# Performance work log

Hardware: AMD Instinct MI355X
Metric: run time of the kernel (lower is better)

The kernel has to match this reference:

```python
import jax, jax.numpy as jnp
import numpy as np

NUM_HEADS = 4

def setup_inputs() -> dict:
    key = jax.random.key(0)
    k1, k2, k3, k4 = jax.random.split(key, 4)
    B, N, D = 8, 768, 2048
    x = jax.random.normal(k1, (B, N, D), dtype=jnp.float32)
    s = 1.0 / np.sqrt(N)
    W_qk = jax.random.normal(k2, (N, N), dtype=jnp.float32) * s
    W_v = jax.random.normal(k3, (N, N), dtype=jnp.float32) * s
    W_out = jax.random.normal(k4, (N, N), dtype=jnp.float32) * s
    return {"x": x, "W_qk": W_qk, "W_v": W_v, "W_out": W_out}

def reference(x, W_qk, W_v, W_out):
    B, N, D = x.shape
    H = NUM_HEADS
    n = N // H
    y = jnp.swapaxes(x, 1, 2)                    # (B, D, N): attention over channels D
    qk = y @ W_qk.T                              # (B, D, N)
    v = y @ W_v.T                                # (B, D, N)
    # to heads: (B, D, N) -> (B, H, D, n)
    qk = jnp.swapaxes(qk.reshape(B, D, H, n), 1, 2)
    v = jnp.swapaxes(v.reshape(B, D, H, n), 1, 2)
    dot = jnp.einsum('bhdn,bhen->bhde', qk, qk)  # (B, H, D, D)
    q2 = jnp.sum(qk * qk, axis=-1)               # (B, H, D)
    # negative squared Euclidean distance logits: 2*q.k - ||q||^2 - ||k||^2
    logits = 2.0 * dot - q2[..., :, None] - q2[..., None, :]
    attn = jax.nn.softmax(logits, axis=-1)
    w = jnp.einsum('bhde,bhen->bhdn', attn, v)   # (B, H, D, n)
    # from heads: (B, H, D, n) -> (B, D, N)
    w = jnp.swapaxes(w, 1, 2).reshape(B, D, N)
    out = w @ W_out.T                            # (B, D, N)
    return jnp.swapaxes(out, 1, 2)               # (B, N, D)
```

## Files before the change

kernel.cpp:

```cpp
#include <hip/hip_runtime.h>
#include <stdint.h>

#define B_  8
#define N_  768
#define D_  2048
#define H_  4
#define HN  192

#define QROW 200
#define VROW 72
#define KTILE_B 25600
#define VTILE_B 27648

typedef unsigned short u16;
typedef float    f32x4 __attribute__((ext_vector_type(4)));
typedef __bf16   bf16x8 __attribute__((ext_vector_type(8)));
typedef uint32_t u32x4 __attribute__((ext_vector_type(4)));
typedef uint32_t u32x2 __attribute__((ext_vector_type(2)));

__device__ __forceinline__ u16 f2bf(float f) {
  uint32_t u = __builtin_bit_cast(uint32_t, f);
  u += 0x7fffu + ((u >> 16) & 1u);
  return (u16)(u >> 16);
}

typedef const __attribute__((address_space(1))) void* gas_ptr;
typedef __attribute__((address_space(3))) void* las_ptr;
__device__ __forceinline__ void gld16(const void* g, void* l) {
  __builtin_amdgcn_global_load_lds((gas_ptr)g, (las_ptr)l, 16, 0, 0);
}

__global__ __launch_bounds__(256) void transpose_x(const float* __restrict__ x,
                                                   u16* __restrict__ xt) {
  __shared__ float tile[64][65];
  const int d0 = blockIdx.x * 64;
  const int n0 = blockIdx.y * 64;
  const int b  = blockIdx.z;
  const int t   = threadIdx.x;
  const int col = t & 63;
  const int rb  = (t >> 6) * 16;
  const float* src = x + ((size_t)b * N_ + n0) * D_ + d0;
  #pragma unroll
  for (int i = 0; i < 16; i++)
    tile[rb + i][col] = src[(size_t)(rb + i) * D_ + col];
  __syncthreads();
  u16* dst = xt + ((size_t)b * D_ + d0) * N_ + n0;
  #pragma unroll
  for (int i = 0; i < 16; i++)
    dst[(size_t)(rb + i) * N_ + col] = f2bf(tile[col][rb + i]);
}

__global__ __launch_bounds__(256) void cvt_w(const float* __restrict__ a,
                                             const float* __restrict__ b,
                                             const float* __restrict__ c,
                                             u16* __restrict__ oa,
                                             u16* __restrict__ ob,
                                             u16* __restrict__ oc) {
  const float* src = (blockIdx.y == 0) ? a : ((blockIdx.y == 1) ? b : c);
  u16*         dst = (blockIdx.y == 0) ? oa : ((blockIdx.y == 1) ? ob : oc);
  const int i = (blockIdx.x * 256 + threadIdx.x) * 4;
  f32x4 v = *(const f32x4*)(src + i);
  u16 tmp[4];
  #pragma unroll
  for (int j = 0; j < 4; j++) tmp[j] = f2bf(v[j]);
  *(u32x2*)(dst + i) = *(u32x2*)tmp;
}

__global__ __launch_bounds__(256) void zero_q2(float* __restrict__ q2) {
  q2[blockIdx.x * 256 + threadIdx.x] = 0.f;
}

__global__ __launch_bounds__(256, 2) void qkv_gemm(const u16* __restrict__ xt,
                                                   const u16* __restrict__ wqk,
                                                   const u16* __restrict__ wv,
                                                   u16* __restrict__ qkb,
                                                   u16* __restrict__ vtb,
                                                   float* __restrict__ q2) {
  const int b     = blockIdx.z;
  const int dtile = blockIdx.x;
  const int d0    = dtile * 128;
  const int j0    = blockIdx.y * 128;
  const int tid  = threadIdx.x;
  const int wave = tid >> 6, lane = tid & 63;
  const int l15  = lane & 15, quad = lane >> 4;
  const int wm = wave >> 1, wn = wave & 1;

  __shared__ u16 At[128 * 32];
  __shared__ u16 Bq[128 * 32];
  __shared__ u16 Bv[128 * 32];

  const f32x4 fz = {0.f, 0.f, 0.f, 0.f};
  f32x4 accq[4][4];
  f32x4 accv[4][4];
  #pragma unroll
  for (int i = 0; i < 4; i++)
    #pragma unroll
    for (int j = 0; j < 4; j++) { accq[i][j] = fz; accv[i][j] = fz; }

  const int srow  = tid >> 2;
  const int sbyte = (tid & 3) * 16;
  const u16* ax = xt  + ((size_t)b * D_ + d0 + srow) * N_;
  const u16* bq = wqk + (size_t)(j0 + srow) * N_;
  const u16* bv = wv  + (size_t)(j0 + srow) * N_;

  for (int k0 = 0; k0 < N_; k0 += 32) {
    __syncthreads();
    #pragma unroll
    for (int c = 0; c < 2; c++) {
      gld16((const char*)(ax + (size_t)c * 64 * N_ + k0) + sbyte,
            (char*)At + c * 4096 + tid * 16);
      gld16((const char*)(bq + (size_t)c * 64 * N_ + k0) + sbyte,
            (char*)Bq + c * 4096 + tid * 16);
      gld16((const char*)(bv + (size_t)c * 64 * N_ + k0) + sbyte,
            (char*)Bv + c * 4096 + tid * 16);
    }
    __syncthreads();

    bf16x8 Af[4];
    #pragma unroll
    for (int mi = 0; mi < 4; mi++)
      Af[mi] = *(const bf16x8*)&At[(wm * 64 + mi * 16 + l15) * 32 + quad * 8];
    #pragma unroll
    for (int ni = 0; ni < 4; ni++) {
      bf16x8 Bqf = *(const bf16x8*)&Bq[(wn * 64 + ni * 16 + l15) * 32 + quad * 8];
      bf16x8 Bvf = *(const bf16x8*)&Bv[(wn * 64 + ni * 16 + l15) * 32 + quad * 8];
      #pragma unroll
      for (int mi = 0; mi < 4; mi++) {
        accq[ni][mi] = __builtin_amdgcn_mfma_f32_16x16x32_bf16(Bqf, Af[mi], accq[ni][mi], 0, 0, 0);
        accv[mi][ni] = __builtin_amdgcn_mfma_f32_16x16x32_bf16(Af[mi], Bvf, accv[mi][ni], 0, 0, 0);
      }
    }
  }

  const int h_w  = (j0 + wn * 64) / HN;
  const int jn_w = (j0 + wn * 64) % HN;
  const size_t bh = (size_t)b * H_ + h_w;

  #pragma unroll
  for (int md = 0; md < 4; md++) {
    float s = 0.f;
    #pragma unroll
    for (int nj = 0; nj < 4; nj++)
      #pragma unroll
      for (int r = 0; r < 4; r++) { float v = accq[nj][md][r]; s += v * v; }
    s += __shfl_xor(s, 16, 64);
    s += __shfl_xor(s, 32, 64);
    if (quad == 0)
      atomicAdd(&q2[bh * D_ + d0 + wm * 64 + md * 16 + l15], s);
  }

  u16* qtbase = qkb + bh * (size_t)(D_ * QROW);
  #pragma unroll
  for (int md = 0; md < 4; md++) {
    const size_t dro = (size_t)(d0 + wm * 64 + md * 16 + l15) * QROW;
    #pragma unroll
    for (int nj = 0; nj < 4; nj++) {
      u16 tmp[4];
      #pragma unroll
      for (int r = 0; r < 4; r++) tmp[r] = f2bf(accq[nj][md][r]);
      *(u32x2*)(qtbase + dro + jn_w + nj * 16 + quad * 4) = *(u32x2*)tmp;
    }
  }

  const int etile = dtile * 2 + wm;
  u16* vtbase = vtb + bh * (size_t)(32 * HN * VROW) + (size_t)etile * (HN * VROW);
  #pragma unroll
  for (int ni = 0; ni < 4; ni++) {
    const size_t jro = (size_t)(jn_w + ni * 16 + l15) * VROW;
    #pragma unroll
    for (int mi = 0; mi < 4; mi++) {
      u16 tmp[4];
      #pragma unroll
      for (int r = 0; r < 4; r++) tmp[r] = f2bf(accv[mi][ni][r]);
      *(u32x2*)(vtbase + jro + mi * 16 + quad * 4) = *(u32x2*)tmp;
    }
  }
}

__global__ __launch_bounds__(256, 2) void attn_kernel(const u16* __restrict__ qkb,
                                                      const u16* __restrict__ vtb,
                                                      const float* __restrict__ q2,
                                                      u16* __restrict__ wbuf) {
  const int bid  = blockIdx.x;
  const int bh   = (bid & 7) * 4 + (bid >> 7);
  const int dblk = (bid >> 3) & 15;
  const int b = bh >> 2, h = bh & 3;
  const int tid  = threadIdx.x;
  const int wave = tid >> 6, lane = tid & 63;
  const int l15  = lane & 15, quad = lane >> 4;

  __shared__ u16 Klds[64 * QROW];
  __shared__ u16 Vlds[HN * VROW];
  __shared__ u16 Plds[4][32][VROW];
  __shared__ float rsl[4][32];

  const u16* kg = qkb + (size_t)bh * (D_ * QROW);
  const u16* vg = vtb + (size_t)bh * (32 * HN * VROW);
  const float* q2g = q2 + (size_t)bh * D_;

  bf16x8 Qf[2][6];
  {
    const u16* qrow = kg + (size_t)(dblk * 128 + wave * 32 + l15) * QROW + quad * 8;
    #pragma unroll
    for (int nt = 0; nt < 2; nt++)
      #pragma unroll
      for (int f = 0; f < 6; f++)
        Qf[nt][f] = *(const bf16x8*)(qrow + (size_t)nt * 16 * QROW + f * 32);
  }
  float cd[2];
  cd[0] = q2g[dblk * 128 + wave * 32 + l15];
  cd[1] = q2g[dblk * 128 + wave * 32 + 16 + l15];

  const f32x4 fz = {0.f, 0.f, 0.f, 0.f};
  f32x4 O[2][12];
  #pragma unroll
  for (int mt = 0; mt < 2; mt++)
    #pragma unroll
    for (int c = 0; c < 12; c++) O[mt][c] = fz;
  float rsp[2] = {0.f, 0.f};

  for (int t = 0; t < 32; t++) {
    __syncthreads();
    {
      const char* ks = (const char*)kg + (size_t)t * KTILE_B;
      char* kd = (char*)Klds;
      for (int c = wave; c < 25; c += 4)
        gld16(ks + c * 1024 + lane * 16, kd + c * 1024 + lane * 16);
      const char* vs = (const char*)vg + (size_t)t * VTILE_B;
      char* vd = (char*)Vlds;
      for (int c = wave; c < 27; c += 4)
        gld16(vs + c * 1024 + lane * 16, vd + c * 1024 + lane * 16);
    }
    __syncthreads();

    #pragma unroll
    for (int et = 0; et < 4; et++) {
      bf16x8 Kf[6];
      #pragma unroll
      for (int f = 0; f < 6; f++)
        Kf[f] = *(const bf16x8*)&Klds[(et * 16 + l15) * QROW + f * 32 + quad * 8];
      f32x4 S0 = fz, S1 = fz;
      #pragma unroll
      for (int f = 0; f < 6; f++) {
        S0 = __builtin_amdgcn_mfma_f32_16x16x32_bf16(Kf[f], Qf[0][f], S0, 0, 0, 0);
        S1 = __builtin_amdgcn_mfma_f32_16x16x32_bf16(Kf[f], Qf[1][f], S1, 0, 0, 0);
      }
      const f32x4 ce = *(const f32x4*)&q2g[t * 64 + et * 16 + quad * 4];
      u16 pk0[4], pk1[4];
      #pragma unroll
      for (int r = 0; r < 4; r++) {
        float p0 = __expf(__builtin_fmaf(S0[r], 2.f, -(ce[r] + cd[0])));
        float p1 = __expf(__builtin_fmaf(S1[r], 2.f, -(ce[r] + cd[1])));
        rsp[0] += p0; rsp[1] += p1;
        pk0[r] = f2bf(p0); pk1[r] = f2bf(p1);
      }
      *(u32x2*)&Plds[wave][l15][et * 16 + quad * 4]      = *(u32x2*)pk0;
      *(u32x2*)&Plds[wave][16 + l15][et * 16 + quad * 4] = *(u32x2*)pk1;
    }

    #pragma unroll
    for (int kk = 0; kk < 2; kk++) {
      bf16x8 Pf0 = *(const bf16x8*)&Plds[wave][l15][kk * 32 + quad * 8];
      bf16x8 Pf1 = *(const bf16x8*)&Plds[wave][16 + l15][kk * 32 + quad * 8];
      #pragma unroll
      for (int c = 0; c < 12; c++) {
        bf16x8 Vf = *(const bf16x8*)&Vlds[(c * 16 + l15) * VROW + kk * 32 + quad * 8];
        O[0][c] = __builtin_amdgcn_mfma_f32_16x16x32_bf16(Pf0, Vf, O[0][c], 0, 0, 0);
        O[1][c] = __builtin_amdgcn_mfma_f32_16x16x32_bf16(Pf1, Vf, O[1][c], 0, 0, 0);
      }
    }
  }

  #pragma unroll
  for (int nt = 0; nt < 2; nt++) {
    float s = rsp[nt];
    s += __shfl_xor(s, 16, 64);
    s += __shfl_xor(s, 32, 64);
    if (quad == 0) rsl[wave][nt * 16 + l15] = s;
  }
  __builtin_amdgcn_s_waitcnt(0);
  #pragma unroll
  for (int mt = 0; mt < 2; mt++)
    #pragma unroll
    for (int r = 0; r < 4; r++) {
      const float inv = 1.f / rsl[wave][mt * 16 + quad * 4 + r];
      const int d = dblk * 128 + wave * 32 + mt * 16 + quad * 4 + r;
      u16* wrow = wbuf + ((size_t)b * D_ + d) * N_ + h * HN;
      #pragma unroll
      for (int c = 0; c < 12; c++)
        wrow[c * 16 + l15] = f2bf(O[mt][c][r] * inv);
    }
}

__global__ __launch_bounds__(256, 2) void out_gemm(const u16* __restrict__ wbuf,
                                                   const u16* __restrict__ wout,
                                                   float* __restrict__ outp) {
  const int b  = blockIdx.z;
  const int d0 = blockIdx.x * 128;
  const int i0 = blockIdx.y * 128;
  const int tid  = threadIdx.x;
  const int wave = tid >> 6, lane = tid & 63;
  const int l15  = lane & 15, quad = lane >> 4;
  const int wm = wave >> 1, wn = wave & 1;

  __shared__ u16 At[128 * 32];
  __shared__ u16 Bt[128 * 32];

  const f32x4 fz = {0.f, 0.f, 0.f, 0.f};
  f32x4 acc[4][4];
  #pragma unroll
  for (int i = 0; i < 4; i++)
    #pragma unroll
    for (int j = 0; j < 4; j++) acc[i][j] = fz;

  const int srow  = tid >> 2;
  const int sbyte = (tid & 3) * 16;
  const u16* ax = wbuf + ((size_t)b * D_ + d0 + srow) * N_;
  const u16* bw = wout + (size_t)(i0 + srow) * N_;

  for (int k0 = 0; k0 < N_; k0 += 32) {
    __syncthreads();
    #pragma unroll
    for (int c = 0; c < 2; c++) {
      gld16((const char*)(ax + (size_t)c * 64 * N_ + k0) + sbyte,
            (char*)At + c * 4096 + tid * 16);
      gld16((const char*)(bw + (size_t)c * 64 * N_ + k0) + sbyte,
            (char*)Bt + c * 4096 + tid * 16);
    }
    __syncthreads();

    bf16x8 Af[4];
    #pragma unroll
    for (int mi = 0; mi < 4; mi++)
      Af[mi] = *(const bf16x8*)&At[(wm * 64 + mi * 16 + l15) * 32 + quad * 8];
    #pragma unroll
    for (int ni = 0; ni < 4; ni++) {
      bf16x8 Bf = *(const bf16x8*)&Bt[(wn * 64 + ni * 16 + l15) * 32 + quad * 8];
      #pragma unroll
      for (int mi = 0; mi < 4; mi++)
        acc[mi][ni] = __builtin_amdgcn_mfma_f32_16x16x32_bf16(Af[mi], Bf, acc[mi][ni], 0, 0, 0);
    }
  }

  #pragma unroll
  for (int ni = 0; ni < 4; ni++) {
    float* orow = outp + ((size_t)b * N_ + i0 + wn * 64 + ni * 16 + l15) * D_
                + d0 + wm * 64 + quad * 4;
    #pragma unroll
    for (int mi = 0; mi < 4; mi++)
      *(f32x4*)(orow + mi * 16) = acc[mi][ni];
  }
}

extern "C" void kernel_launch(void* const* d_in, const int* in_sizes, int n_in,
                              void* d_out, int out_size, void* d_ws, size_t ws_size,
                              hipStream_t stream) {
  (void)in_sizes; (void)n_in; (void)out_size; (void)ws_size;
  const float* x    = (const float*)d_in[0];
  const float* Wqk  = (const float*)d_in[1];
  const float* Wv   = (const float*)d_in[2];
  const float* Wout = (const float*)d_in[3];
  float* outp = (float*)d_out;

  char* ws = (char*)d_ws;
  size_t off = 0;
  u16* xt   = (u16*)(ws + off); off += (size_t)B_ * D_ * N_ * 2;
  u16* qkb  = (u16*)(ws + off); off += (size_t)B_ * H_ * D_ * QROW * 2;
  u16* vtb  = (u16*)(ws + off); off += (size_t)B_ * H_ * 32 * HN * VROW * 2;
  float* q2 = (float*)(ws + off); off += (size_t)B_ * H_ * D_ * 4;
  u16* wqk_bf  = (u16*)(ws + off); off += (size_t)N_ * N_ * 2;
  u16* wv_bf   = (u16*)(ws + off); off += (size_t)N_ * N_ * 2;
  u16* wout_bf = (u16*)(ws + off); off += (size_t)N_ * N_ * 2;
  u16* wbuf = xt;

  transpose_x<<<dim3(D_ / 64, N_ / 64, B_), 256, 0, stream>>>(x, xt);
  cvt_w<<<dim3((N_ * N_) / (256 * 4), 3), 256, 0, stream>>>(Wqk, Wv, Wout, wqk_bf, wv_bf, wout_bf);
  zero_q2<<<dim3((B_ * H_ * D_) / 256), 256, 0, stream>>>(q2);
  qkv_gemm<<<dim3(D_ / 128, N_ / 128, B_), 256, 0, stream>>>(xt, wqk_bf, wv_bf, qkb, vtb, q2);
  attn_kernel<<<dim3((D_ / 128) * B_ * H_), 256, 0, stream>>>(qkb, vtb, q2, wbuf);
  out_gemm<<<dim3(D_ / 128, N_ / 128, B_), 256, 0, stream>>>(wbuf, wout_bf, outp);
}
```

Measured before the change: 303.8 us.

## Compute softmax row sums via MFMA with ones, use exp2 and hardware bf16 converts

Folds log2(e) into the precomputed squared norms and the logit scale, so the attention kernel can call the native exp2 instruction instead of expf. The per-lane running row-sum and its shuffle/LDS reduction are replaced by an extra MFMA of P against an all-ones fragment, which yields row sums directly in accumulator layout. Software bf16 rounding is replaced by hardware casts, and s_setprio is placed around the MFMA blocks to favour matrix-issue scheduling. This adds two MFMAs per k-step and computes the row sum from bf16-rounded probabilities, which slightly changes numerics.

```diff
diff --git a/kernel.cpp b/kernel.cpp
--- a/kernel.cpp
+++ b/kernel.cpp
@@ -12,16 +12,18 @@
 #define KTILE_B 25600
 #define VTILE_B 27648
 
+#define LOG2E 1.4426950408889634f
+#define C2    2.8853901617f
+
 typedef unsigned short u16;
 typedef float    f32x4 __attribute__((ext_vector_type(4)));
 typedef __bf16   bf16x8 __attribute__((ext_vector_type(8)));
+typedef __bf16   bf16x4 __attribute__((ext_vector_type(4)));
 typedef uint32_t u32x4 __attribute__((ext_vector_type(4)));
 typedef uint32_t u32x2 __attribute__((ext_vector_type(2)));
 
 __device__ __forceinline__ u16 f2bf(float f) {
-  uint32_t u = __builtin_bit_cast(uint32_t, f);
-  u += 0x7fffu + ((u >> 16) & 1u);
-  return (u16)(u >> 16);
+  return __builtin_bit_cast(u16, (__bf16)f);
 }
 
 typedef const __attribute__((address_space(1))) void* gas_ptr;
@@ -146,7 +148,7 @@
     s += __shfl_xor(s, 16, 64);
     s += __shfl_xor(s, 32, 64);
     if (quad == 0)
-      atomicAdd(&q2[bh * D_ + d0 + wm * 64 + md * 16 + l15], s);
+      atomicAdd(&q2[bh * D_ + d0 + wm * 64 + md * 16 + l15], s * LOG2E);
   }
 
   u16* qtbase = qkb + bh * (size_t)(D_ * QROW);
@@ -155,10 +157,10 @@
     const size_t dro = (size_t)(d0 + wm * 64 + md * 16 + l15) * QROW;
     #pragma unroll
     for (int nj = 0; nj < 4; nj++) {
-      u16 tmp[4];
-      #pragma unroll
-      for (int r = 0; r < 4; r++) tmp[r] = f2bf(accq[nj][md][r]);
-      *(u32x2*)(qtbase + dro + jn_w + nj * 16 + quad * 4) = *(u32x2*)tmp;
+      bf16x4 tmp;
+      #pragma unroll
+      for (int r = 0; r < 4; r++) tmp[r] = (__bf16)accq[nj][md][r];
+      *(bf16x4*)(qtbase + dro + jn_w + nj * 16 + quad * 4) = tmp;
     }
   }
 
@@ -169,10 +171,10 @@
     const size_t jro = (size_t)(jn_w + ni * 16 + l15) * VROW;
     #pragma unroll
     for (int mi = 0; mi < 4; mi++) {
-      u16 tmp[4];
-      #pragma unroll
-      for (int r = 0; r < 4; r++) tmp[r] = f2bf(accv[mi][ni][r]);
-      *(u32x2*)(vtbase + jro + mi * 16 + quad * 4) = *(u32x2*)tmp;
+      bf16x4 tmp;
+      #pragma unroll
+      for (int r = 0; r < 4; r++) tmp[r] = (__bf16)accv[mi][ni][r];
+      *(bf16x4*)(vtbase + jro + mi * 16 + quad * 4) = tmp;
     }
   }
 }
@@ -192,7 +194,6 @@
   __shared__ u16 Klds[64 * QROW];
   __shared__ u16 Vlds[HN * VROW];
   __shared__ u16 Plds[4][32][VROW];
-  __shared__ float rsl[4][32];
 
   const u16* kg = qkb + (size_t)bh * (D_ * QROW);
   const u16* vg = vtb + (size_t)bh * (32 * HN * VROW);
@@ -211,13 +212,19 @@
   cd[0] = q2g[dblk * 128 + wave * 32 + l15];
   cd[1] = q2g[dblk * 128 + wave * 32 + 16 + l15];
 
+  bf16x8 OnesF;
+  #pragma unroll
+  for (int j = 0; j < 8; j++) OnesF[j] = (__bf16)1.0f;
+
   const f32x4 fz = {0.f, 0.f, 0.f, 0.f};
   f32x4 O[2][12];
-  #pragma unroll
-  for (int mt = 0; mt < 2; mt++)
+  f32x4 Or[2];
+  #pragma unroll
+  for (int mt = 0; mt < 2; mt++) {
+    Or[mt] = fz;
     #pragma unroll
     for (int c = 0; c < 12; c++) O[mt][c] = fz;
-  float rsp[2] = {0.f, 0.f};
+  }
 
   for (int t = 0; t < 32; t++) {
     __syncthreads();
@@ -240,50 +247,48 @@
       for (int f = 0; f < 6; f++)
         Kf[f] = *(const bf16x8*)&Klds[(et * 16 + l15) * QROW + f * 32 + quad * 8];
       f32x4 S0 = fz, S1 = fz;
+      __builtin_amdgcn_s_setprio(1);
       #pragma unroll
       for (int f = 0; f < 6; f++) {
         S0 = __builtin_amdgcn_mfma_f32_16x16x32_bf16(Kf[f], Qf[0][f], S0, 0, 0, 0);
         S1 = __builtin_amdgcn_mfma_f32_16x16x32_bf16(Kf[f], Qf[1][f], S1, 0, 0, 0);
       }
+      __builtin_amdgcn_s_setprio(0);
       const f32x4 ce = *(const f32x4*)&q2g[t * 64 + et * 16 + quad * 4];
-      u16 pk0[4], pk1[4];
+      bf16x4 pb0, pb1;
       #pragma unroll
       for (int r = 0; r < 4; r++) {
-        float p0 = __expf(__builtin_fmaf(S0[r], 2.f, -(ce[r] + cd[0])));
-        float p1 = __expf(__builtin_fmaf(S1[r], 2.f, -(ce[r] + cd[1])));
-        rsp[0] += p0; rsp[1] += p1;
-        pk0[r] = f2bf(p0); pk1[r] = f2bf(p1);
+        float p0 = __builtin_amdgcn_exp2f(__builtin_fmaf(S0[r], C2, -(ce[r] + cd[0])));
+        float p1 = __builtin_amdgcn_exp2f(__builtin_fmaf(S1[r], C2, -(ce[r] + cd[1])));
+        pb0[r] = (__bf16)p0;
+        pb1[r] = (__bf16)p1;
       }
-      *(u32x2*)&Plds[wave][l15][et * 16 + quad * 4]      = *(u32x2*)pk0;
-      *(u32x2*)&Plds[wave][16 + l15][et * 16 + quad * 4] = *(u32x2*)pk1;
+      *(bf16x4*)&Plds[wave][l15][et * 16 + quad * 4]      = pb0;
+      *(bf16x4*)&Plds[wave][16 + l15][et * 16 + quad * 4] = pb1;
     }
 
     #pragma unroll
     for (int kk = 0; kk < 2; kk++) {
       bf16x8 Pf0 = *(const bf16x8*)&Plds[wave][l15][kk * 32 + quad * 8];
       bf16x8 Pf1 = *(const bf16x8*)&Plds[wave][16 + l15][kk * 32 + quad * 8];
+      __builtin_amdgcn_s_setprio(1);
       #pragma unroll
       for (int c = 0; c < 12; c++) {
         bf16x8 Vf = *(const bf16x8*)&Vlds[(c * 16 + l15) * VROW + kk * 32 + quad * 8];
         O[0][c] = __builtin_amdgcn_mfma_f32_16x16x32_bf16(Pf0, Vf, O[0][c], 0, 0, 0);
         O[1][c] = __builtin_amdgcn_mfma_f32_16x16x32_bf16(Pf1, Vf, O[1][c], 0, 0, 0);
       }
-    }
-  }
-
-  #pragma unroll
-  for (int nt = 0; nt < 2; nt++) {
-    float s = rsp[nt];
-    s += __shfl_xor(s, 16, 64);
-    s += __shfl_xor(s, 32, 64);
-    if (quad == 0) rsl[wave][nt * 16 + l15] = s;
-  }
-  __builtin_amdgcn_s_waitcnt(0);
+      Or[0] = __builtin_amdgcn_mfma_f32_16x16x32_bf16(Pf0, OnesF, Or[0], 0, 0, 0);
+      Or[1] = __builtin_amdgcn_mfma_f32_16x16x32_bf16(Pf1, OnesF, Or[1], 0, 0, 0);
+      __builtin_amdgcn_s_setprio(0);
+    }
+  }
+
   #pragma unroll
   for (int mt = 0; mt < 2; mt++)
     #pragma unroll
     for (int r = 0; r < 4; r++) {
-      const float inv = 1.f / rsl[wave][mt * 16 + quad * 4 + r];
+      const float inv = __builtin_amdgcn_rcpf(Or[mt][r]);
       const int d = dblk * 128 + wave * 32 + mt * 16 + quad * 4 + r;
       u16* wrow = wbuf + ((size_t)b * D_ + d) * N_ + h * HN;
       #pragma unroll
```

Measured after the change: 298.9 us. No clear change (-1.6%).
